# Kernel tuning notes

Measured on AMD Instinct MI355X. Metric: run time of the kernel, lower is better.

Reference implementation:

```python
import jax, jax.numpy as jnp
import numpy as np

H = 1024          # hidden_size
V = 50257         # output_size (vocab)
L = 100           # max_length


def setup_inputs() -> dict:
    key = jax.random.key(0)
    ks = jax.random.split(key, 16)
    s = 0.02
    return {
        "input": jax.random.randint(ks[0], (1,), 0, V, dtype=jnp.int64),
        "hidden": jax.random.normal(ks[1], (1, 1, H), dtype=jnp.float32),
        "encoder_outputs": jax.random.normal(ks[2], (L, H), dtype=jnp.float32),
        # parameters
        "emb": jax.random.normal(ks[3], (V, H), dtype=jnp.float32) * s,
        "attn_W": jax.random.normal(ks[4], (L, 2 * H), dtype=jnp.float32) * s,
        "attn_b": jnp.zeros((L,), dtype=jnp.float32),
        "comb_W": jax.random.normal(ks[5], (H, 2 * H), dtype=jnp.float32) * s,
        "comb_b": jnp.zeros((H,), dtype=jnp.float32),
        "W_ih": jax.random.normal(ks[6], (3 * H, H), dtype=jnp.float32) * s,
        "W_hh": jax.random.normal(ks[7], (3 * H, H), dtype=jnp.float32) * s,
        "b_ih": jnp.zeros((3 * H,), dtype=jnp.float32),
        "b_hh": jnp.zeros((3 * H,), dtype=jnp.float32),
        "out_W": jax.random.normal(ks[8], (V, H), dtype=jnp.float32) * s,
        "out_b": jnp.zeros((V,), dtype=jnp.float32),
    }


def reference(input, hidden, encoder_outputs, emb, attn_W, attn_b,
              comb_W, comb_b, W_ih, W_hh, b_ih, b_hh, out_W, out_b):
    # embedding lookup -> [1, H]; dropout is identity at inference
    embedded = emb[input].reshape(1, H)
    h0 = hidden[0]                                     # [1, H]
    # Bahdanau-style attention over fixed max_length positions
    attn_logits = jnp.concatenate([embedded, h0], axis=1) @ attn_W.T + attn_b
    attn_weights = jax.nn.softmax(attn_logits, axis=1)  # [1, L]
    context = attn_weights @ encoder_outputs            # [1, H]
    # combine + relu
    x = jnp.concatenate([embedded, context], axis=1) @ comb_W.T + comb_b
    x = jax.nn.relu(x)                                  # [1, H]
    # single-step GRU (PyTorch gate order: r, z, n)
    gi = x @ W_ih.T + b_ih                              # [1, 3H]
    gh = h0 @ W_hh.T + b_hh                             # [1, 3H]
    i_r, i_z, i_n = jnp.split(gi, 3, axis=1)
    h_r, h_z, h_n = jnp.split(gh, 3, axis=1)
    r = jax.nn.sigmoid(i_r + h_r)
    z = jax.nn.sigmoid(i_z + h_z)
    n = jnp.tanh(i_n + r * h_n)
    h_new = (1.0 - z) * n + z * h0                      # [1, H]
    # output projection + log_softmax
    logits = h_new @ out_W.T + out_b                    # [1, V]
    out = jax.nn.log_softmax(logits, axis=1)
    return out, h_new[None], attn_weights
```

## Files before the change

### kernel.cpp

```cpp
#include <hip/hip_runtime.h>
#include <math.h>

#define H   1024
#define H2  2048
#define L   100
#define V   50257

#define WS_ATT   0
#define WS_CTX   128
#define WS_X     1280
#define WS_HNEW  2304
#define WS_C     3328

__device__ __forceinline__ float wave_reduce_sum(float v) {
#pragma unroll
    for (int off = 32; off > 0; off >>= 1) v += __shfl_down(v, off);
    return v;
}

__global__ void k_attn_logits(const int* __restrict__ tok,
                              const float* __restrict__ hidden,
                              const float* __restrict__ emb,
                              const float* __restrict__ attn_W,
                              const float* __restrict__ attn_b,
                              float* __restrict__ ws) {
    const int l = blockIdx.x;
    const int t = threadIdx.x;
    const float* __restrict__ row = attn_W + (size_t)l * H2;
    const float* __restrict__ e   = emb + (size_t)tok[0] * H;
    float acc = 0.f;
#pragma unroll
    for (int base = 0; base < H2; base += 1024) {
        int i = base + t * 4;
        float4 w = *(const float4*)(row + i);
        const float* __restrict__ src = (i < H) ? (e + i) : (hidden + (i - H));
        float4 v = *(const float4*)src;
        acc += w.x * v.x + w.y * v.y + w.z * v.z + w.w * v.w;
    }
    acc = wave_reduce_sum(acc);
    __shared__ float sh[4];
    if ((t & 63) == 0) sh[t >> 6] = acc;
    __syncthreads();
    if (t == 0) ws[WS_ATT + l] = sh[0] + sh[1] + sh[2] + sh[3] + attn_b[l];
}

__global__ void k_attn_softmax(float* __restrict__ ws, float* __restrict__ out) {
    const int t = threadIdx.x;
    __shared__ float sh[128];
    float v = (t < L) ? ws[WS_ATT + t] : -INFINITY;
    sh[t] = v;
    __syncthreads();
    for (int s = 64; s > 0; s >>= 1) {
        if (t < s) sh[t] = fmaxf(sh[t], sh[t + s]);
        __syncthreads();
    }
    float m = sh[0];
    __syncthreads();
    float e = (t < L) ? expf(v - m) : 0.f;
    sh[t] = e;
    __syncthreads();
    for (int s = 64; s > 0; s >>= 1) {
        if (t < s) sh[t] += sh[t + s];
        __syncthreads();
    }
    float denom = sh[0];
    if (t < L) {
        float w = e / denom;
        ws[WS_ATT + t] = w;
        out[V + H + t] = w;
    }
}

__global__ void k_context(const float* __restrict__ enc, float* __restrict__ ws) {
    const int h = blockIdx.x * 128 + threadIdx.x;
    float acc = 0.f;
#pragma unroll 4
    for (int l = 0; l < L; ++l) acc += ws[WS_ATT + l] * enc[(size_t)l * H + h];
    ws[WS_CTX + h] = acc;
}

__global__ void k_combine(const int* __restrict__ tok,
                          const float* __restrict__ emb,
                          const float* __restrict__ comb_W,
                          const float* __restrict__ comb_b,
                          float* __restrict__ ws) {
    const int t = threadIdx.x;
    const int wave = t >> 6, lane = t & 63;
    const int j = blockIdx.x * 4 + wave;
    const float* __restrict__ e   = emb + (size_t)tok[0] * H;
    const float* __restrict__ ctx = ws + WS_CTX;
    const float* __restrict__ row = comb_W + (size_t)j * H2;
    float acc = 0.f;
#pragma unroll
    for (int it = 0; it < 8; ++it) {
        int i = it * 256 + lane * 4;
        float4 w = *(const float4*)(row + i);
        const float* __restrict__ src = (i < H) ? (e + i) : (ctx + (i - H));
        float4 v = *(const float4*)src;
        acc += w.x * v.x + w.y * v.y + w.z * v.z + w.w * v.w;
    }
    acc = wave_reduce_sum(acc);
    if (lane == 0) ws[WS_X + j] = fmaxf(acc + comb_b[j], 0.f);
}

__global__ void k_gru(const float* __restrict__ hidden,
                      const float* __restrict__ W_ih,
                      const float* __restrict__ W_hh,
                      const float* __restrict__ b_ih,
                      const float* __restrict__ b_hh,
                      float* __restrict__ ws,
                      float* __restrict__ out) {
    const int j = blockIdx.x;
    const int t = threadIdx.x;
    const int w = t >> 6, lane = t & 63;
    const float* __restrict__ vec = (w < 3) ? (ws + WS_X) : hidden;
    const float* __restrict__ row = (w < 3)
        ? (W_ih + ((size_t)w * H + j) * H)
        : (W_hh + ((size_t)(w - 3) * H + j) * H);
    float acc = 0.f;
#pragma unroll
    for (int it = 0; it < 4; ++it) {
        int i = it * 256 + lane * 4;
        float4 a = *(const float4*)(row + i);
        float4 v = *(const float4*)(vec + i);
        acc += a.x * v.x + a.y * v.y + a.z * v.z + a.w * v.w;
    }
    acc = wave_reduce_sum(acc);
    __shared__ float sh[6];
    if (lane == 0) sh[w] = acc;
    __syncthreads();
    if (t == 0) {
        float ir  = sh[0] + b_ih[j];
        float iz  = sh[1] + b_ih[H + j];
        float inn = sh[2] + b_ih[2 * H + j];
        float hr  = sh[3] + b_hh[j];
        float hz  = sh[4] + b_hh[H + j];
        float hn  = sh[5] + b_hh[2 * H + j];
        float r = 1.f / (1.f + expf(-(ir + hr)));
        float z = 1.f / (1.f + expf(-(iz + hz)));
        float n = tanhf(inn + r * hn);
        float hnew = (1.f - z) * n + z * hidden[j];
        out[V + j]       = hnew;
        ws[WS_HNEW + j]  = hnew;
    }
}

__global__ void k_out_gemv(const float* __restrict__ out_W,
                           const float* __restrict__ out_b,
                           const float* __restrict__ ws,
                           float* __restrict__ out) {
    __shared__ float sh[H];
    const int t = threadIdx.x;
    *(float4*)(sh + t * 4) = *(const float4*)(ws + WS_HNEW + t * 4);
    __syncthreads();
    const int wave = t >> 6, lane = t & 63;
    const int v = blockIdx.x * 4 + wave;
    if (v >= V) return;
    const float* __restrict__ row = out_W + (size_t)v * H;
    float acc = 0.f;
#pragma unroll
    for (int it = 0; it < 4; ++it) {
        int i = it * 256 + lane * 4;
        float4 a = *(const float4*)(row + i);
        float4 b = *(const float4*)(sh + i);
        acc += a.x * b.x + a.y * b.y + a.z * b.z + a.w * b.w;
    }
    acc = wave_reduce_sum(acc);
    if (lane == 0) out[v] = acc + out_b[v];
}

__global__ void k_lse(const float* __restrict__ out, float* __restrict__ ws) {
    const int t = threadIdx.x;
    float m = -INFINITY, s = 0.f;
    const int V4 = V & ~3;
    for (int v = t * 4; v < V4; v += 4096) {
        float4 x = *(const float4*)(out + v);
        float lm = fmaxf(fmaxf(x.x, x.y), fmaxf(x.z, x.w));
        float ls = expf(x.x - lm) + expf(x.y - lm) + expf(x.z - lm) + expf(x.w - lm);
        if (lm > m) { s = s * expf(m - lm) + ls; m = lm; }
        else        { s += ls * expf(lm - m); }
    }
    for (int v = V4 + t; v < V; v += 1024) {
        float x = out[v];
        if (x > m) { s = s * expf(m - x) + 1.f; m = x; }
        else       { s += expf(x - m); }
    }
#pragma unroll
    for (int off = 32; off > 0; off >>= 1) {
        float m2 = __shfl_down(m, off);
        float s2 = __shfl_down(s, off);
        float M = fmaxf(m, m2);
        s = s * expf(m - M) + s2 * expf(m2 - M);
        m = M;
    }
    __shared__ float shm[16], shs[16];
    const int wave = t >> 6, lane = t & 63;
    if (lane == 0) { shm[wave] = m; shs[wave] = s; }
    __syncthreads();
    if (t == 0) {
        float M = shm[0], S = shs[0];
        for (int i = 1; i < 16; ++i) {
            float M2 = fmaxf(M, shm[i]);
            S = S * expf(M - M2) + shs[i] * expf(shm[i] - M2);
            M = M2;
        }
        ws[WS_C] = M + logf(S);
    }
}

__global__ void k_sub(float* __restrict__ out, const float* __restrict__ ws) {
    const int v = blockIdx.x * 256 + threadIdx.x;
    if (v < V) out[v] -= ws[WS_C];
}

extern "C" void kernel_launch(void* const* d_in, const int* in_sizes, int n_in,
                              void* d_out, int out_size, void* d_ws, size_t ws_size,
                              hipStream_t stream) {
    const int*   tok    = (const int*)d_in[0];
    const float* hidden = (const float*)d_in[1];
    const float* enc    = (const float*)d_in[2];
    const float* emb    = (const float*)d_in[3];
    const float* attn_W = (const float*)d_in[4];
    const float* attn_b = (const float*)d_in[5];
    const float* comb_W = (const float*)d_in[6];
    const float* comb_b = (const float*)d_in[7];
    const float* W_ih   = (const float*)d_in[8];
    const float* W_hh   = (const float*)d_in[9];
    const float* b_ih   = (const float*)d_in[10];
    const float* b_hh   = (const float*)d_in[11];
    const float* out_W  = (const float*)d_in[12];
    const float* out_b  = (const float*)d_in[13];
    float* out = (float*)d_out;
    float* ws  = (float*)d_ws;

    k_attn_logits<<<L, 256, 0, stream>>>(tok, hidden, emb, attn_W, attn_b, ws);
    k_attn_softmax<<<1, 128, 0, stream>>>(ws, out);
    k_context<<<8, 128, 0, stream>>>(enc, ws);
    k_combine<<<256, 256, 0, stream>>>(tok, emb, comb_W, comb_b, ws);
    k_gru<<<H, 384, 0, stream>>>(hidden, W_ih, W_hh, b_ih, b_hh, ws, out);
    k_out_gemv<<<(V + 3) / 4, 256, 0, stream>>>(out_W, out_b, ws, out);
    k_lse<<<1, 1024, 0, stream>>>(out, ws);
    k_sub<<<(V + 255) / 256, 256, 0, stream>>>(out, ws);
}
```

Before: 434.7 us.

## Fuse attention softmax into context, emit per-block LSE partials from output GEMV

The attention softmax is merged into the context kernel, with each block recomputing the softmax redundantly, which removes one launch. The output GEMV now handles 16 rows per block, four per wave, with nontemporal loads of out_W. Each block also writes a partial max and sum-of-exp, so the single-block LSE kernel reduces about 3.1K partials instead of rereading all 50K logits. The cost is a serial max/sum by thread 0 in every GEMV block and a larger workspace footprint.

Result: faster. 420.2 us (-3.3%).

```diff
diff --git a/kernel.cpp b/kernel.cpp
--- a/kernel.cpp
+++ b/kernel.cpp
@@ -6,11 +6,17 @@
 #define L   100
 #define V   50257
 
+#define ROWS_PB 16
+#define NBLK_OUT ((V + ROWS_PB - 1) / ROWS_PB)
+
 #define WS_ATT   0
 #define WS_CTX   128
 #define WS_X     1280
 #define WS_HNEW  2304
-#define WS_C     3328
+#define WS_PART  3328
+#define WS_C     9728
+
+typedef float floatx4 __attribute__((ext_vector_type(4)));
 
 __device__ __forceinline__ float wave_reduce_sum(float v) {
 #pragma unroll
@@ -44,38 +50,39 @@
     if (t == 0) ws[WS_ATT + l] = sh[0] + sh[1] + sh[2] + sh[3] + attn_b[l];
 }
 
-__global__ void k_attn_softmax(float* __restrict__ ws, float* __restrict__ out) {
-    const int t = threadIdx.x;
-    __shared__ float sh[128];
+__global__ void k_ctx(const float* __restrict__ enc,
+                      float* __restrict__ ws,
+                      float* __restrict__ out) {
+    const int t = threadIdx.x;
+    __shared__ float sl[128];
+    __shared__ float shw[L];
     float v = (t < L) ? ws[WS_ATT + t] : -INFINITY;
-    sh[t] = v;
+    sl[t] = v;
     __syncthreads();
     for (int s = 64; s > 0; s >>= 1) {
-        if (t < s) sh[t] = fmaxf(sh[t], sh[t + s]);
+        if (t < s) sl[t] = fmaxf(sl[t], sl[t + s]);
         __syncthreads();
     }
-    float m = sh[0];
+    float m = sl[0];
     __syncthreads();
     float e = (t < L) ? expf(v - m) : 0.f;
-    sh[t] = e;
+    sl[t] = e;
     __syncthreads();
     for (int s = 64; s > 0; s >>= 1) {
-        if (t < s) sh[t] += sh[t + s];
+        if (t < s) sl[t] += sl[t + s];
         __syncthreads();
     }
-    float denom = sh[0];
+    float denom = sl[0];
     if (t < L) {
         float w = e / denom;
-        ws[WS_ATT + t] = w;
-        out[V + H + t] = w;
-    }
-}
-
-__global__ void k_context(const float* __restrict__ enc, float* __restrict__ ws) {
-    const int h = blockIdx.x * 128 + threadIdx.x;
+        shw[t] = w;
+        if (blockIdx.x == 0) out[V + H + t] = w;
+    }
+    __syncthreads();
+    const int h = blockIdx.x * 128 + t;
     float acc = 0.f;
 #pragma unroll 4
-    for (int l = 0; l < L; ++l) acc += ws[WS_ATT + l] * enc[(size_t)l * H + h];
+    for (int l = 0; l < L; ++l) acc += shw[l] * enc[(size_t)l * H + h];
     ws[WS_CTX + h] = acc;
 }
 
@@ -140,50 +147,87 @@
         float z = 1.f / (1.f + expf(-(iz + hz)));
         float n = tanhf(inn + r * hn);
         float hnew = (1.f - z) * n + z * hidden[j];
-        out[V + j]       = hnew;
-        ws[WS_HNEW + j]  = hnew;
+        out[V + j]      = hnew;
+        ws[WS_HNEW + j] = hnew;
     }
 }
 
 __global__ void k_out_gemv(const float* __restrict__ out_W,
                            const float* __restrict__ out_b,
                            const float* __restrict__ ws,
-                           float* __restrict__ out) {
-    __shared__ float sh[H];
-    const int t = threadIdx.x;
-    *(float4*)(sh + t * 4) = *(const float4*)(ws + WS_HNEW + t * 4);
+                           float* __restrict__ out,
+                           float* __restrict__ part) {
+    __shared__ float shv[H];
+    __shared__ float slog[ROWS_PB];
+    const int t = threadIdx.x;
+    *(float4*)(shv + t * 4) = *(const float4*)(ws + WS_HNEW + t * 4);
     __syncthreads();
     const int wave = t >> 6, lane = t & 63;
-    const int v = blockIdx.x * 4 + wave;
-    if (v >= V) return;
-    const float* __restrict__ row = out_W + (size_t)v * H;
-    float acc = 0.f;
-#pragma unroll
-    for (int it = 0; it < 4; ++it) {
-        int i = it * 256 + lane * 4;
-        float4 a = *(const float4*)(row + i);
-        float4 b = *(const float4*)(sh + i);
-        acc += a.x * b.x + a.y * b.y + a.z * b.z + a.w * b.w;
-    }
-    acc = wave_reduce_sum(acc);
-    if (lane == 0) out[v] = acc + out_b[v];
-}
-
-__global__ void k_lse(const float* __restrict__ out, float* __restrict__ ws) {
+    const int r0 = blockIdx.x * ROWS_PB + wave * 4;
+    const float* __restrict__ base = out_W + (size_t)r0 * H;
+    float acc0 = 0.f, acc1 = 0.f, acc2 = 0.f, acc3 = 0.f;
+    if (r0 + 3 < V) {
+#pragma unroll
+        for (int it = 0; it < 4; ++it) {
+            const int i = it * 256 + lane * 4;
+            float4 b = *(const float4*)(shv + i);
+            floatx4 a0 = __builtin_nontemporal_load((const floatx4*)(base + i));
+            floatx4 a1 = __builtin_nontemporal_load((const floatx4*)(base + H + i));
+            floatx4 a2 = __builtin_nontemporal_load((const floatx4*)(base + 2 * H + i));
+            floatx4 a3 = __builtin_nontemporal_load((const floatx4*)(base + 3 * H + i));
+            acc0 += a0.x * b.x + a0.y * b.y + a0.z * b.z + a0.w * b.w;
+            acc1 += a1.x * b.x + a1.y * b.y + a1.z * b.z + a1.w * b.w;
+            acc2 += a2.x * b.x + a2.y * b.y + a2.z * b.z + a2.w * b.w;
+            acc3 += a3.x * b.x + a3.y * b.y + a3.z * b.z + a3.w * b.w;
+        }
+    } else {
+        for (int it = 0; it < 4; ++it) {
+            const int i = it * 256 + lane * 4;
+            float4 b = *(const float4*)(shv + i);
+            if (r0 + 0 < V) { float4 a = *(const float4*)(base + i);
+                acc0 += a.x * b.x + a.y * b.y + a.z * b.z + a.w * b.w; }
+            if (r0 + 1 < V) { float4 a = *(const float4*)(base + H + i);
+                acc1 += a.x * b.x + a.y * b.y + a.z * b.z + a.w * b.w; }
+            if (r0 + 2 < V) { float4 a = *(const float4*)(base + 2 * H + i);
+                acc2 += a.x * b.x + a.y * b.y + a.z * b.z + a.w * b.w; }
+            if (r0 + 3 < V) { float4 a = *(const float4*)(base + 3 * H + i);
+                acc3 += a.x * b.x + a.y * b.y + a.z * b.z + a.w * b.w; }
+        }
+    }
+    acc0 = wave_reduce_sum(acc0);
+    acc1 = wave_reduce_sum(acc1);
+    acc2 = wave_reduce_sum(acc2);
+    acc3 = wave_reduce_sum(acc3);
+    if (lane == 0) {
+        float lg[4] = {acc0, acc1, acc2, acc3};
+#pragma unroll
+        for (int r = 0; r < 4; ++r) {
+            int row = r0 + r;
+            float l = (row < V) ? lg[r] + out_b[row] : -INFINITY;
+            if (row < V) out[row] = l;
+            slog[wave * 4 + r] = l;
+        }
+    }
+    __syncthreads();
+    if (t == 0) {
+        float m = slog[0];
+#pragma unroll
+        for (int i = 1; i < ROWS_PB; ++i) m = fmaxf(m, slog[i]);
+        float s = 0.f;
+#pragma unroll
+        for (int i = 0; i < ROWS_PB; ++i) s += expf(slog[i] - m);
+        part[2 * blockIdx.x]     = m;
+        part[2 * blockIdx.x + 1] = s;
+    }
+}
+
+__global__ void k_lse(const float* __restrict__ part, float* __restrict__ ws) {
     const int t = threadIdx.x;
     float m = -INFINITY, s = 0.f;
-    const int V4 = V & ~3;
-    for (int v = t * 4; v < V4; v += 4096) {
-        float4 x = *(const float4*)(out + v);
-        float lm = fmaxf(fmaxf(x.x, x.y), fmaxf(x.z, x.w));
-        float ls = expf(x.x - lm) + expf(x.y - lm) + expf(x.z - lm) + expf(x.w - lm);
-        if (lm > m) { s = s * expf(m - lm) + ls; m = lm; }
-        else        { s += ls * expf(lm - m); }
-    }
-    for (int v = V4 + t; v < V; v += 1024) {
-        float x = out[v];
-        if (x > m) { s = s * expf(m - x) + 1.f; m = x; }
-        else       { s += expf(x - m); }
+    for (int i = t; i < NBLK_OUT; i += 256) {
+        float pm = part[2 * i], ps = part[2 * i + 1];
+        if (pm > m) { s = s * expf(m - pm) + ps; m = pm; }
+        else        { s += ps * expf(pm - m); }
     }
 #pragma unroll
     for (int off = 32; off > 0; off >>= 1) {
@@ -193,13 +237,13 @@
         s = s * expf(m - M) + s2 * expf(m2 - M);
         m = M;
     }
-    __shared__ float shm[16], shs[16];
+    __shared__ float shm[4], shs[4];
     const int wave = t >> 6, lane = t & 63;
     if (lane == 0) { shm[wave] = m; shs[wave] = s; }
     __syncthreads();
     if (t == 0) {
         float M = shm[0], S = shs[0];
-        for (int i = 1; i < 16; ++i) {
+        for (int i = 1; i < 4; ++i) {
             float M2 = fmaxf(M, shm[i]);
             S = S * expf(M - M2) + shs[i] * expf(shm[i] - M2);
             M = M2;
@@ -234,11 +278,10 @@
     float* ws  = (float*)d_ws;
 
     k_attn_logits<<<L, 256, 0, stream>>>(tok, hidden, emb, attn_W, attn_b, ws);
-    k_attn_softmax<<<1, 128, 0, stream>>>(ws, out);
-    k_context<<<8, 128, 0, stream>>>(enc, ws);
+    k_ctx<<<8, 128, 0, stream>>>(enc, ws, out);
     k_combine<<<256, 256, 0, stream>>>(tok, emb, comb_W, comb_b, ws);
     k_gru<<<H, 384, 0, stream>>>(hidden, W_ih, W_hh, b_ih, b_hh, ws, out);
-    k_out_gemv<<<(V + 3) / 4, 256, 0, stream>>>(out_W, out_b, ws, out);
-    k_lse<<<1, 1024, 0, stream>>>(out, ws);
+    k_out_gemv<<<NBLK_OUT, 256, 0, stream>>>(out_W, out_b, ws, out, ws + WS_PART);
+    k_lse<<<1, 256, 0, stream>>>(ws + WS_PART, ws);
     k_sub<<<(V + 255) / 256, 256, 0, stream>>>(out, ws);
 }
```
